# Performance work log

Measured on AMD Instinct MI355X. Metric: run time of the kernel, lower is better.

Reference implementation:

```python
import jax, jax.numpy as jnp
import numpy as np

EMB = 64  # emb_dim
T = 4     # message-passing steps


def setup_inputs() -> dict:
    key = jax.random.key(0)
    ks = jax.random.split(key, 9)
    B, N = 32, 1024
    graph = jax.random.uniform(ks[0], (B, N, N), jnp.float32)   # dense adjacency/weights
    Xv = jax.random.normal(ks[1], (B, N, 1), jnp.float32)       # per-vertex scalar feature
    s = lambda k, shp: (jax.random.normal(k, shp, jnp.float32) * 0.05)
    return {
        "graph": graph,
        "Xv": Xv,
        "W1": s(ks[2], (EMB, 1)),        # Linear(1, emb) no bias, torch layout [out, in]
        "W2": s(ks[3], (EMB, EMB)),
        "W3": s(ks[4], (EMB, EMB)),
        "W4": s(ks[5], (EMB, 1)),
        "W5": s(ks[6], (1, 2 * EMB)),
        "W6": s(ks[7], (EMB, EMB)),
        "W7": s(ks[8], (EMB, EMB)),
    }


def reference(graph, Xv, W1, W2, W3, W4, W5, W6, W7):
    B, N = Xv.shape[0], Xv.shape[1]
    # v1 = W1(Xv): [B,N,1] @ [1,EMB] -> [B,N,EMB]
    v1 = Xv @ W1.T
    # Original: v3 = W3(sum_j W4(graph[...,None])). W4 is linear (no bias), so
    # sum_j W4(g_ij) == W4(sum_j g_ij) -- exact by linearity, avoids [B,N,N,EMB] temp.
    deg = jnp.sum(graph, axis=2, keepdims=True)        # [B,N,1]
    v3 = (deg @ W4.T) @ W3.T                           # [B,N,EMB]
    base = v1 + v3                                     # loop-invariant part
    emb = jnp.zeros((B, N, EMB), dtype=Xv.dtype)
    for _ in range(T):
        neighbor_sum = jnp.einsum('bij,bjd->bid', graph, emb)  # bmm aggregation
        emb = jax.nn.relu(base + neighbor_sum @ W2.T)
    emb_sum = jnp.sum(emb, axis=1)                     # [B,EMB]
    # v6.repeat(1,N).view(B,N,EMB) == broadcast the per-graph vector to every vertex
    v6 = jnp.broadcast_to((emb_sum @ W6.T)[:, None, :], (B, N, EMB))
    v7 = emb @ W7.T
    ct = jax.nn.relu(jnp.concatenate([v6, v7], axis=2))  # [B,N,2*EMB]
    return (ct @ W5.T)[..., 0]                            # [B,N]
```

## Files before the change

### kernel.cpp

```cpp
#include <hip/hip_runtime.h>
#include <stdint.h>

#define NV 1024
#define EMB 64

typedef __attribute__((ext_vector_type(8))) short bf16x8;
typedef __attribute__((ext_vector_type(4))) float f32x4;

__device__ __forceinline__ unsigned short f2b(float f) {
  unsigned int u = __builtin_bit_cast(unsigned int, f);
  u += 0x7fffu + ((u >> 16) & 1u);
  return (unsigned short)(u >> 16);
}
__device__ __forceinline__ float b2f(unsigned short s) {
  unsigned int u = ((unsigned int)s) << 16;
  return __builtin_bit_cast(float, u);
}

__device__ __forceinline__ void gll16(void* lds, const void* gsrc) {
  __builtin_amdgcn_global_load_lds(
      (const __attribute__((address_space(1))) unsigned int*)gsrc,
      (__attribute__((address_space(3))) unsigned int*)lds, 16, 0, 0);
}

__device__ __forceinline__ void swz(int j, int& b, int& mb) {
  const int xcd = j & 7, s = j >> 3;
  b = xcd + 8 * (s >> 4);
  mb = s & 15;
}

__global__ __launch_bounds__(256) void k_prep(
    const float* __restrict__ graph, const float* __restrict__ Xv,
    const float* __restrict__ W1, const float* __restrict__ W3,
    const float* __restrict__ W4,
    unsigned short* __restrict__ G16, float* __restrict__ degp,
    float* __restrict__ w34g, unsigned short* __restrict__ embT)
{
  __shared__ float w34s[EMB];
  __shared__ __align__(16) unsigned short ebT[EMB][68];
  const int tid = threadIdx.x;
  int b, mb; swz(blockIdx.x, b, mb);
  if (tid < EMB) {
    float s = 0.f;
    const float* w3r = W3 + tid * EMB;
#pragma unroll
    for (int k = 0; k < EMB; ++k) s += w3r[k] * W4[k];
    w34s[tid] = s;
    if (blockIdx.x == 0) w34g[tid] = s;
  }
  __syncthreads();
  const int wv = tid >> 6, lane = tid & 63;
  const float w1v = W1[lane];
  const float w34v = w34s[lane];
  for (int i = 0; i < 16; ++i) {
    const int rloc = wv * 16 + i;
    const int row = mb * 64 + rloc;
    const float4* gr = (const float4*)(graph + ((size_t)b * NV + row) * NV);
    float part = 0.f;
    ushort4 outp[4];
#pragma unroll
    for (int c = 0; c < 4; ++c) {
      float4 v = gr[c * 64 + lane];
      part += (v.x + v.y) + (v.z + v.w);
      outp[c].x = f2b(v.x); outp[c].y = f2b(v.y);
      outp[c].z = f2b(v.z); outp[c].w = f2b(v.w);
    }
    ushort4* g16r = (ushort4*)(G16 + ((size_t)b * NV + row) * NV);
#pragma unroll
    for (int c = 0; c < 4; ++c) g16r[c * 64 + lane] = outp[c];
#pragma unroll
    for (int d = 1; d < 64; d <<= 1) part += __shfl_xor(part, d);
    const float deg = part;
    if (lane == 0) degp[b * NV + row] = deg;
    const float xv = Xv[b * NV + row];
    const float bs = xv * w1v + deg * w34v;
    ebT[lane][rloc] = f2b(fmaxf(bs, 0.f));
  }
  __syncthreads();
  const int e = tid >> 2, q = tid & 3;
  ushort4* dst = (ushort4*)(embT + ((size_t)(b * EMB + e)) * NV + mb * 64 + q * 16);
  const ushort4* srcr = (const ushort4*)(&ebT[e][q * 16]);
#pragma unroll
  for (int c = 0; c < 4; ++c) dst[c] = srcr[c];
}

template <int LAST>
__global__ __launch_bounds__(256, 4) void k_step(
    const unsigned short* __restrict__ G16,
    const unsigned short* __restrict__ embin,
    unsigned short* __restrict__ embout,
    const float* __restrict__ W2, const float* __restrict__ W1,
    const float* __restrict__ w34g, const float* __restrict__ Xv,
    const float* __restrict__ degp, float* __restrict__ esum_ws)
{
  __shared__ __align__(16) char ldsbuf[49152];
  __shared__ float esl[EMB];
  const int tid = threadIdx.x;
  const int lane = tid & 63;
  const int wv = tid >> 6;
  int b, mb; swz(blockIdx.x, b, mb);
  const int wm = wv >> 1, wn = wv & 1;
  const int l15 = lane & 15, l4 = lane >> 4;

  bf16x8 w2f[2][2];
  float w1e[2], w34e[2];
#pragma unroll
  for (int e16 = 0; e16 < 2; ++e16) {
    const int eg = wn * 32 + e16 * 16 + l15;
    w1e[e16] = W1[eg];
    w34e[e16] = w34g[eg];
#pragma unroll
    for (int kk = 0; kk < 2; ++kk) {
      const float* src = W2 + eg * 64 + kk * 32 + l4 * 8;
      bf16x8 f;
#pragma unroll
      for (int j = 0; j < 8; ++j) f[j] = (short)f2b(src[j]);
      w2f[e16][kk] = f;
    }
  }
  if (LAST && tid < EMB) esl[tid] = 0.f;

  f32x4 acc[2][2] = {};
  const size_t gbase = ((size_t)b * NV + mb * 64) * NV;
  const size_t ebase = (size_t)b * EMB * NV;

  auto STAGE = [&](int bufi, int kt) {
    char* Ad = ldsbuf + bufi * 16384;
    char* Bd = Ad + 8192;
#pragma unroll
    for (int i = 0; i < 2; ++i) {
      const int cc = i * 256 + tid;
      const int lrow = cc >> 3, lcg = cc & 7;
      const int gcg = lcg ^ (lrow & 7);
      gll16(Ad + (i * 256 + wv * 64) * 16,
            G16 + gbase + (size_t)lrow * NV + kt * 64 + gcg * 8);
    }
#pragma unroll
    for (int i = 0; i < 2; ++i) {
      const int cc = i * 256 + tid;
      const int er = cc >> 3, lcg = cc & 7;
      const int gcg = lcg ^ (er & 7);
      gll16(Bd + (i * 256 + wv * 64) * 16,
            embin + ebase + (size_t)er * NV + kt * 64 + gcg * 8);
    }
  };

  STAGE(0, 0);
  STAGE(1, 1);
  for (int kt = 0; kt < 16; ++kt) {
    if (kt < 14) {
      STAGE((kt + 2) % 3, kt + 2);
      asm volatile("s_waitcnt vmcnt(8)" ::: "memory");
    } else if (kt == 14) {
      asm volatile("s_waitcnt vmcnt(4)" ::: "memory");
    } else {
      asm volatile("s_waitcnt vmcnt(0)" ::: "memory");
    }
    __builtin_amdgcn_s_barrier();
    asm volatile("" ::: "memory");
    const char* At = ldsbuf + (kt % 3) * 16384;
    const char* Bt = At + 8192;
#pragma unroll
    for (int kk = 0; kk < 2; ++kk) {
      bf16x8 af[2], bfr[2];
      const int gq = kk * 4 + l4;
#pragma unroll
      for (int m16 = 0; m16 < 2; ++m16) {
        const int row = wm * 32 + m16 * 16 + l15;
        af[m16] = *(const bf16x8*)(At + row * 128 + ((gq ^ (row & 7)) << 4));
      }
#pragma unroll
      for (int n16 = 0; n16 < 2; ++n16) {
        const int er = wn * 32 + n16 * 16 + l15;
        bfr[n16] = *(const bf16x8*)(Bt + er * 128 + ((gq ^ (er & 7)) << 4));
      }
#pragma unroll
      for (int m16 = 0; m16 < 2; ++m16)
#pragma unroll
        for (int n16 = 0; n16 < 2; ++n16)
          acc[m16][n16] = __builtin_amdgcn_mfma_f32_16x16x32_bf16(
              af[m16], bfr[n16], acc[m16][n16], 0, 0, 0);
    }
    asm volatile("" ::: "memory");
    __builtin_amdgcn_s_barrier();
  }

  char* St = ldsbuf;
#pragma unroll
  for (int m16 = 0; m16 < 2; ++m16)
#pragma unroll
    for (int n16 = 0; n16 < 2; ++n16)
#pragma unroll
      for (int r = 0; r < 4; ++r) {
        const int m = wm * 32 + m16 * 16 + l4 * 4 + r;
        const int n = wn * 32 + n16 * 16 + l15;
        const int addr = m * 128 + (((n >> 3) ^ (m & 7)) << 4) + (n & 7) * 2;
        *(unsigned short*)(St + addr) = f2b(acc[m16][n16][r]);
      }
  __syncthreads();

  f32x4 acc2[2][2] = {};
#pragma unroll
  for (int kk = 0; kk < 2; ++kk) {
    bf16x8 sa[2];
    const int gq = kk * 4 + l4;
#pragma unroll
    for (int m16 = 0; m16 < 2; ++m16) {
      const int row = wm * 32 + m16 * 16 + l15;
      sa[m16] = *(const bf16x8*)(St + row * 128 + ((gq ^ (row & 7)) << 4));
    }
#pragma unroll
    for (int m16 = 0; m16 < 2; ++m16)
#pragma unroll
      for (int e16 = 0; e16 < 2; ++e16)
        acc2[m16][e16] = __builtin_amdgcn_mfma_f32_16x16x32_bf16(
            sa[m16], w2f[e16][kk], acc2[m16][e16], 0, 0, 0);
  }

#pragma unroll
  for (int m16 = 0; m16 < 2; ++m16) {
    const int ml0 = wm * 32 + m16 * 16 + l4 * 4;
    const int m0 = mb * 64 + ml0;
    float xv4[4], dg4[4];
#pragma unroll
    for (int r = 0; r < 4; ++r) {
      xv4[r] = Xv[b * NV + m0 + r];
      dg4[r] = degp[b * NV + m0 + r];
    }
#pragma unroll
    for (int e16 = 0; e16 < 2; ++e16) {
      const int eg = wn * 32 + e16 * 16 + l15;
      ushort4 pk;
      unsigned short* pks = (unsigned short*)&pk;
      float evs = 0.f;
#pragma unroll
      for (int r = 0; r < 4; ++r) {
        const float bs = xv4[r] * w1e[e16] + dg4[r] * w34e[e16];
        const float val = fmaxf(acc2[m16][e16][r] + bs, 0.f);
        pks[r] = f2b(val);
        evs += val;
      }
      *(ushort4*)(embout + ((size_t)(b * EMB + eg)) * NV + m0) = pk;
      if (LAST) atomicAdd(&esl[eg], evs);
    }
  }
  if (LAST) {
    __syncthreads();
    if (tid < EMB) atomicAdd(&esum_ws[b * EMB + tid], esl[tid]);
  }
}

__global__ __launch_bounds__(256) void k_out(
    const unsigned short* __restrict__ embT, const float* __restrict__ W7,
    const float* __restrict__ W5, const float* __restrict__ W6,
    const float* __restrict__ esum_ws, float* __restrict__ out)
{
  __shared__ __align__(16) unsigned short et[EMB][256];
  __shared__ float s6l;
  const int tid = threadIdx.x;
  const int b = blockIdx.x >> 2;
  const int n0 = (blockIdx.x & 3) * 256;
#pragma unroll
  for (int i = 0; i < 8; ++i) {
    const int c = i * 256 + tid;
    const int k = c >> 5, off = (c & 31) * 8;
    *(uint4*)&et[k][off] =
        *(const uint4*)(embT + ((size_t)(b * EMB + k)) * NV + n0 + off);
  }
  if (tid < EMB) {
    const float* es = esum_ws + b * EMB;
    float v6 = 0.f;
    const float* w6r = W6 + tid * EMB;
#pragma unroll
    for (int k = 0; k < EMB; ++k) v6 += w6r[k] * es[k];
    float c = W5[tid] * fmaxf(v6, 0.f);
#pragma unroll
    for (int d = 1; d < 64; d <<= 1) c += __shfl_xor(c, d);
    if (tid == 0) s6l = c;
  }
  __syncthreads();
  float ev[64];
#pragma unroll
  for (int k = 0; k < 64; ++k) ev[k] = b2f(et[k][tid]);
  float s7 = 0.f;
  for (int e = 0; e < 64; ++e) {
    const float* w7r = W7 + e * 64;
    float a = 0.f;
#pragma unroll
    for (int k = 0; k < 64; ++k) a += ev[k] * w7r[k];
    s7 += W5[64 + e] * fmaxf(a, 0.f);
  }
  out[b * NV + n0 + tid] = s6l + s7;
}

extern "C" void kernel_launch(void* const* d_in, const int* in_sizes, int n_in,
                              void* d_out, int out_size, void* d_ws, size_t ws_size,
                              hipStream_t stream) {
  const float* graph = (const float*)d_in[0];
  const float* Xv = (const float*)d_in[1];
  const float* W1 = (const float*)d_in[2];
  const float* W2 = (const float*)d_in[3];
  const float* W3 = (const float*)d_in[4];
  const float* W4 = (const float*)d_in[5];
  const float* W5 = (const float*)d_in[6];
  const float* W6 = (const float*)d_in[7];
  const float* W7 = (const float*)d_in[8];
  float* out = (float*)d_out;
  char* ws = (char*)d_ws;

  unsigned short* G16 = (unsigned short*)ws;
  unsigned short* embA = (unsigned short*)(ws + (64u << 20));
  unsigned short* embB = (unsigned short*)(ws + (68u << 20));
  float* degp = (float*)(ws + (72u << 20));
  float* w34g = (float*)(ws + (72u << 20) + (128u << 10));
  float* esum_ws = (float*)(ws + (72u << 20) + (130u << 10));

  hipMemsetAsync(esum_ws, 0, 32 * EMB * sizeof(float), stream);
  k_prep<<<512, 256, 0, stream>>>(graph, Xv, W1, W3, W4, G16, degp, w34g, embA);
  k_step<0><<<512, 256, 0, stream>>>(G16, embA, embB, W2, W1, w34g, Xv, degp, esum_ws);
  k_step<0><<<512, 256, 0, stream>>>(G16, embB, embA, W2, W1, w34g, Xv, degp, esum_ws);
  k_step<1><<<512, 256, 0, stream>>>(G16, embA, embB, W2, W1, w34g, Xv, degp, esum_ws);
  k_out<<<128, 256, 0, stream>>>(embB, W7, W5, W6, esum_ws, out);
}
```

Measured before the change: 296.8 us.

## Use 512-thread blocks and 4-stage LDS pipeline in step kernel

Doubles the step kernel's block size from 256 to 512 threads (8 waves). Each wave now computes a 16x32 output tile instead of 32x32, and each thread issues one global-to-LDS load per operand per stage. The LDS ring buffer grows from three to four stages (64 KB) with deeper prefetch. This aims to hide memory latency of the bandwidth-bound adjacency matmul through more waves and more loads in flight, at the cost of lower per-wave reuse and more LDS per block, which may limit occupancy.

```diff
diff --git a/kernel.cpp b/kernel.cpp
--- a/kernel.cpp
+++ b/kernel.cpp
@@ -85,7 +85,7 @@
 }
 
 template <int LAST>
-__global__ __launch_bounds__(256, 4) void k_step(
+__global__ __launch_bounds__(512, 4) void k_step(
     const unsigned short* __restrict__ G16,
     const unsigned short* __restrict__ embin,
     unsigned short* __restrict__ embout,
@@ -93,13 +93,14 @@
     const float* __restrict__ w34g, const float* __restrict__ Xv,
     const float* __restrict__ degp, float* __restrict__ esum_ws)
 {
-  __shared__ __align__(16) char ldsbuf[49152];
+  __shared__ __align__(16) char ldsbuf[65536];
   __shared__ float esl[EMB];
   const int tid = threadIdx.x;
   const int lane = tid & 63;
   const int wv = tid >> 6;
   int b, mb; swz(blockIdx.x, b, mb);
-  const int wm = wv >> 1, wn = wv & 1;
+  const int wm = wv >> 1;
+  const int wn = wv & 1;
   const int l15 = lane & 15, l4 = lane >> 4;
 
   bf16x8 w2f[2][2];
@@ -120,66 +121,48 @@
   }
   if (LAST && tid < EMB) esl[tid] = 0.f;
 
-  f32x4 acc[2][2] = {};
+  f32x4 acc[2] = {};
   const size_t gbase = ((size_t)b * NV + mb * 64) * NV;
   const size_t ebase = (size_t)b * EMB * NV;
 
+  const int lrow = tid >> 3;
+  const int gcg = (tid & 7) ^ (lrow & 7);
+  const size_t asrc = gbase + (size_t)lrow * NV + gcg * 8;
+  const size_t bsrc = ebase + (size_t)lrow * NV + gcg * 8;
+
   auto STAGE = [&](int bufi, int kt) {
     char* Ad = ldsbuf + bufi * 16384;
-    char* Bd = Ad + 8192;
-#pragma unroll
-    for (int i = 0; i < 2; ++i) {
-      const int cc = i * 256 + tid;
-      const int lrow = cc >> 3, lcg = cc & 7;
-      const int gcg = lcg ^ (lrow & 7);
-      gll16(Ad + (i * 256 + wv * 64) * 16,
-            G16 + gbase + (size_t)lrow * NV + kt * 64 + gcg * 8);
-    }
-#pragma unroll
-    for (int i = 0; i < 2; ++i) {
-      const int cc = i * 256 + tid;
-      const int er = cc >> 3, lcg = cc & 7;
-      const int gcg = lcg ^ (er & 7);
-      gll16(Bd + (i * 256 + wv * 64) * 16,
-            embin + ebase + (size_t)er * NV + kt * 64 + gcg * 8);
-    }
+    gll16(Ad + wv * 1024, G16 + asrc + kt * 64);
+    gll16(Ad + 8192 + wv * 1024, embin + bsrc + kt * 64);
   };
 
-  STAGE(0, 0);
-  STAGE(1, 1);
+  STAGE(0, 0); STAGE(1, 1); STAGE(2, 2);
   for (int kt = 0; kt < 16; ++kt) {
-    if (kt < 14) {
-      STAGE((kt + 2) % 3, kt + 2);
-      asm volatile("s_waitcnt vmcnt(8)" ::: "memory");
+    if (kt < 13) {
+      STAGE((kt + 3) & 3, kt + 3);
+      asm volatile("s_waitcnt vmcnt(6)" ::: "memory");
+    } else if (kt == 13) {
+      asm volatile("s_waitcnt vmcnt(4)" ::: "memory");
     } else if (kt == 14) {
-      asm volatile("s_waitcnt vmcnt(4)" ::: "memory");
+      asm volatile("s_waitcnt vmcnt(2)" ::: "memory");
     } else {
       asm volatile("s_waitcnt vmcnt(0)" ::: "memory");
     }
     __builtin_amdgcn_s_barrier();
     asm volatile("" ::: "memory");
-    const char* At = ldsbuf + (kt % 3) * 16384;
+    const char* At = ldsbuf + (kt & 3) * 16384;
     const char* Bt = At + 8192;
 #pragma unroll
     for (int kk = 0; kk < 2; ++kk) {
-      bf16x8 af[2], bfr[2];
       const int gq = kk * 4 + l4;
-#pragma unroll
-      for (int m16 = 0; m16 < 2; ++m16) {
-        const int row = wm * 32 + m16 * 16 + l15;
-        af[m16] = *(const bf16x8*)(At + row * 128 + ((gq ^ (row & 7)) << 4));
-      }
+      const int row = wm * 16 + l15;
+      const bf16x8 af = *(const bf16x8*)(At + row * 128 + ((gq ^ (row & 7)) << 4));
 #pragma unroll
       for (int n16 = 0; n16 < 2; ++n16) {
         const int er = wn * 32 + n16 * 16 + l15;
-        bfr[n16] = *(const bf16x8*)(Bt + er * 128 + ((gq ^ (er & 7)) << 4));
+        const bf16x8 bfr = *(const bf16x8*)(Bt + er * 128 + ((gq ^ (er & 7)) << 4));
+        acc[n16] = __builtin_amdgcn_mfma_f32_16x16x32_bf16(af, bfr, acc[n16], 0, 0, 0);
       }
-#pragma unroll
-      for (int m16 = 0; m16 < 2; ++m16)
-#pragma unroll
-        for (int n16 = 0; n16 < 2; ++n16)
-          acc[m16][n16] = __builtin_amdgcn_mfma_f32_16x16x32_bf16(
-              af[m16], bfr[n16], acc[m16][n16], 0, 0, 0);
     }
     asm volatile("" ::: "memory");
     __builtin_amdgcn_s_barrier();
@@ -187,62 +170,51 @@
 
   char* St = ldsbuf;
 #pragma unroll
-  for (int m16 = 0; m16 < 2; ++m16)
-#pragma unroll
-    for (int n16 = 0; n16 < 2; ++n16)
-#pragma unroll
-      for (int r = 0; r < 4; ++r) {
-        const int m = wm * 32 + m16 * 16 + l4 * 4 + r;
-        const int n = wn * 32 + n16 * 16 + l15;
-        const int addr = m * 128 + (((n >> 3) ^ (m & 7)) << 4) + (n & 7) * 2;
-        *(unsigned short*)(St + addr) = f2b(acc[m16][n16][r]);
-      }
-  __syncthreads();
-
-  f32x4 acc2[2][2] = {};
+  for (int n16 = 0; n16 < 2; ++n16)
+#pragma unroll
+    for (int r = 0; r < 4; ++r) {
+      const int m = wm * 16 + l4 * 4 + r;
+      const int n = wn * 32 + n16 * 16 + l15;
+      const int addr = m * 128 + (((n >> 3) ^ (m & 7)) << 4) + (n & 7) * 2;
+      *(unsigned short*)(St + addr) = f2b(acc[n16][r]);
+    }
+  __syncthreads();
+
+  f32x4 acc2[2] = {};
 #pragma unroll
   for (int kk = 0; kk < 2; ++kk) {
-    bf16x8 sa[2];
     const int gq = kk * 4 + l4;
-#pragma unroll
-    for (int m16 = 0; m16 < 2; ++m16) {
-      const int row = wm * 32 + m16 * 16 + l15;
-      sa[m16] = *(const bf16x8*)(St + row * 128 + ((gq ^ (row & 7)) << 4));
-    }
-#pragma unroll
-    for (int m16 = 0; m16 < 2; ++m16)
-#pragma unroll
-      for (int e16 = 0; e16 < 2; ++e16)
-        acc2[m16][e16] = __builtin_amdgcn_mfma_f32_16x16x32_bf16(
-            sa[m16], w2f[e16][kk], acc2[m16][e16], 0, 0, 0);
-  }
-
-#pragma unroll
-  for (int m16 = 0; m16 < 2; ++m16) {
-    const int ml0 = wm * 32 + m16 * 16 + l4 * 4;
-    const int m0 = mb * 64 + ml0;
-    float xv4[4], dg4[4];
+    const int row = wm * 16 + l15;
+    const bf16x8 sa = *(const bf16x8*)(St + row * 128 + ((gq ^ (row & 7)) << 4));
+#pragma unroll
+    for (int e16 = 0; e16 < 2; ++e16)
+      acc2[e16] = __builtin_amdgcn_mfma_f32_16x16x32_bf16(
+          sa, w2f[e16][kk], acc2[e16], 0, 0, 0);
+  }
+
+  const int ml0 = wm * 16 + l4 * 4;
+  const int m0 = mb * 64 + ml0;
+  float xv4[4], dg4[4];
+#pragma unroll
+  for (int r = 0; r < 4; ++r) {
+    xv4[r] = Xv[b * NV + m0 + r];
+    dg4[r] = degp[b * NV + m0 + r];
+  }
+#pragma unroll
+  for (int e16 = 0; e16 < 2; ++e16) {
+    const int eg = wn * 32 + e16 * 16 + l15;
+    ushort4 pk;
+    unsigned short* pks = (unsigned short*)&pk;
+    float evs = 0.f;
 #pragma unroll
     for (int r = 0; r < 4; ++r) {
-      xv4[r] = Xv[b * NV + m0 + r];
-      dg4[r] = degp[b * NV + m0 + r];
-    }
-#pragma unroll
-    for (int e16 = 0; e16 < 2; ++e16) {
-      const int eg = wn * 32 + e16 * 16 + l15;
-      ushort4 pk;
-      unsigned short* pks = (unsigned short*)&pk;
-      float evs = 0.f;
-#pragma unroll
-      for (int r = 0; r < 4; ++r) {
-        const float bs = xv4[r] * w1e[e16] + dg4[r] * w34e[e16];
-        const float val = fmaxf(acc2[m16][e16][r] + bs, 0.f);
-        pks[r] = f2b(val);
-        evs += val;
-      }
-      *(ushort4*)(embout + ((size_t)(b * EMB + eg)) * NV + m0) = pk;
-      if (LAST) atomicAdd(&esl[eg], evs);
-    }
+      const float bs = xv4[r] * w1e[e16] + dg4[r] * w34e[e16];
+      const float val = fmaxf(acc2[e16][r] + bs, 0.f);
+      pks[r] = f2b(val);
+      evs += val;
+    }
+    *(ushort4*)(embout + ((size_t)(b * EMB + eg)) * NV + m0) = pk;
+    if (LAST) atomicAdd(&esl[eg], evs);
   }
   if (LAST) {
     __syncthreads();
@@ -317,8 +289,8 @@
 
   hipMemsetAsync(esum_ws, 0, 32 * EMB * sizeof(float), stream);
   k_prep<<<512, 256, 0, stream>>>(graph, Xv, W1, W3, W4, G16, degp, w34g, embA);
-  k_step<0><<<512, 256, 0, stream>>>(G16, embA, embB, W2, W1, w34g, Xv, degp, esum_ws);
-  k_step<0><<<512, 256, 0, stream>>>(G16, embB, embA, W2, W1, w34g, Xv, degp, esum_ws);
-  k_step<1><<<512, 256, 0, stream>>>(G16, embA, embB, W2, W1, w34g, Xv, degp, esum_ws);
+  k_step<0><<<512, 512, 0, stream>>>(G16, embA, embB, W2, W1, w34g, Xv, degp, esum_ws);
+  k_step<0><<<512, 512, 0, stream>>>(G16, embB, embA, W2, W1, w34g, Xv, degp, esum_ws);
+  k_step<1><<<512, 512, 0, stream>>>(G16, embA, embB, W2, W1, w34g, Xv, degp, esum_ws);
   k_out<<<128, 256, 0, stream>>>(embB, W7, W5, W6, esum_ws, out);
 }
```

New measurement: 301.3 us. About the same (+1.5%).
